# Kernel tuning notes

Measured on AMD Instinct MI355X. Metric: run time of the kernel, lower is better.

## Reference

```python
import jax, jax.numpy as jnp
import numpy as np
import math

DIFF = True   # params['diff'] -> kind='random_walk'
SHIFT = 0.0   # params['shift']
MIN_WINDOW = 10
EPS = 1e-6


def _window_sizes(T):
    ws = []
    cur = math.log10(MIN_WINDOW)
    end = math.log10(T - 1)
    while cur < end:
        w = int(10 ** cur)
        if MIN_WINDOW <= w <= T - 1:
            ws.append(w)
        cur += 0.25
    if T not in ws:
        ws.append(T)
    return sorted(set(ws))


def _hurst_random_walk(x):
    B, T = x.shape
    ws = _window_sizes(T)  # static python list (shapes are static)
    rs_list = []
    for w in ws:
        n = T // w
        seg = x[:, : n * w].reshape(B, n, w)            # (B, n, w)
        d = seg[..., 1:] - seg[..., :-1]                # (B, n, w-1)
        mean_inc = (seg[..., -1] - seg[..., 0]) / (w - 1)
        dev = d - mean_inc[..., None]
        Z = jnp.cumsum(dev, axis=-1)                    # rescaled-range scan
        R = jnp.max(Z, axis=-1) - jnp.min(Z, axis=-1)   # (B, n)
        S = jnp.std(d, axis=-1, ddof=1)                 # unbiased std
        rs_list.append(jnp.mean(R / (S + EPS), axis=-1))
    RS = jnp.stack(rs_list, axis=1)                     # (B, K)
    X = jnp.log10(jnp.asarray(ws, dtype=x.dtype) + EPS) # (K,)
    Y = jnp.log10(RS + EPS)
    Xc = X - jnp.mean(X)
    denom = jnp.sum(Xc * Xc)
    H = jnp.sum((Y - jnp.mean(Y, axis=1, keepdims=True)) * Xc, axis=1) / (denom + EPS)
    H = jnp.where(jnp.isfinite(H), H, jnp.asarray(1.0, x.dtype))
    return H


def setup_inputs() -> dict:
    key = jax.random.key(0)
    x = jax.random.normal(key, (8192, 4096), dtype=jnp.float32)
    return {"x": x}


def reference(x):
    H = _hurst_random_walk(x)
    return (H + SHIFT)[:, None]  # (B, 1)
```

## Files before the change

### kernel.cpp

```cpp
#include <hip/hip_runtime.h>
#include <math.h>
#include <utility>

#define TLEN 4096
#define NW   12
#define BLOCK 256
#define EPSF 1e-6f

typedef float v2f __attribute__((ext_vector_type(2)));

__device__ const float XC_TAB[NW] = {
    -1.3608041f, -1.1303552f, -0.8694424f, -0.6126161f,
    -0.3608041f, -0.1128308f,  0.1388830f,  0.3889322f,
     0.6391959f,  0.8891277f,  1.1391578f,  1.2515558f };
__device__ const float INVN_TAB[NW] = {
    1.0f/409.0f, 1.0f/240.0f, 1.0f/132.0f, 1.0f/73.0f,
    1.0f/40.0f,  1.0f/23.0f,  1.0f/12.0f,  1.0f/7.0f,
    0.25f, 0.5f, 1.0f, 1.0f };
#define INV_DEN 0.11577579f
#define LOG10_2 0.30102999566f

__device__ __forceinline__ float max3f(float a, float b, float c) {
    float r; asm("v_max3_f32 %0, %1, %2, %3" : "=v"(r) : "v"(a), "v"(b), "v"(c)); return r;
}
__device__ __forceinline__ float min3f(float a, float b, float c) {
    float r; asm("v_min3_f32 %0, %1, %2, %3" : "=v"(r) : "v"(a), "v"(b), "v"(c)); return r;
}
__device__ __forceinline__ v2f pk_fma(v2f a, v2f b, v2f c) {
    v2f d; asm("v_pk_fma_f32 %0, %1, %2, %3" : "=v"(d) : "v"(a), "v"(b), "v"(c)); return d;
}
__device__ __forceinline__ v2f pk_add(v2f a, v2f b) {
    v2f d; asm("v_pk_add_f32 %0, %1, %2" : "=v"(d) : "v"(a), "v"(b)); return d;
}

__device__ __forceinline__ float wave_reduce_sum(float v) {
    #pragma unroll
    for (int o = 32; o > 0; o >>= 1) v += __shfl_xor(v, o, 64);
    return v;
}
template<int G>
__device__ __forceinline__ float reduce_leaders(float v) {
    #pragma unroll
    for (int o = G; o < 64; o <<= 1) v += __shfl_xor(v, o, 64);
    return v;
}

template<int FLO, int FHI>
__device__ __forceinline__ float seg_rs2(const float* __restrict__ row,
                                         const float* __restrict__ P4,
                                         int b, int W, float m, float invwm2,
                                         float mx, float mn) {
    float plo = P4[b >> 2];
    if constexpr (FLO > 0) {
        const int k0 = b - FLO;
        #pragma unroll
        for (int t = 0; t < FLO; ++t) {
            float d = row[k0 + t + 1] - row[k0 + t];
            plo = fmaf(d, d, plo);
        }
    }
    const int e = b + W - 1;
    float phi = P4[e >> 2];
    if constexpr (FHI > 0) {
        const int k0 = e - FHI;
        #pragma unroll
        for (int t = 0; t < FHI; ++t) {
            float d = row[k0 + t + 1] - row[k0 + t];
            phi = fmaf(d, d, phi);
        }
    }
    float ss  = phi - plo;
    float var = fmaf(-(float)(W - 1) * m, m, ss) * invwm2;
    float S   = __builtin_amdgcn_sqrtf(fmaxf(var, 0.0f));
    return (mx - mn) * __builtin_amdgcn_rcpf(S + EPSF);
}

template<int LO, int HI, int JB>
__device__ __forceinline__ void chunk_fold(const float4 q, float nm, float& mx, float& mn) {
    if constexpr (LO <= HI) {
        constexpr int NV = HI - LO + 1;
        float v[NV];
        #pragma unroll
        for (int r = 0; r < NV; ++r)
            v[r] = fmaf((float)(JB + LO + r), nm, (&q.x)[LO + r]);
        if constexpr (NV == 1) { mx = fmaxf(mx, v[0]); mn = fminf(mn, v[0]); }
        else if constexpr (NV == 2) { mx = max3f(mx, v[0], v[1]); mn = min3f(mn, v[0], v[1]); }
        else if constexpr (NV == 3) { mx = fmaxf(mx, max3f(v[0], v[1], v[2]));
                                      mn = fminf(mn, min3f(v[0], v[1], v[2])); }
        else { mx = max3f(max3f(mx, v[0], v[1]), v[2], v[3]);
               mn = min3f(min3f(mn, v[0], v[1]), v[2], v[3]); }
    }
}

__device__ __forceinline__ float w10_task(const float* __restrict__ row,
                                          const float* __restrict__ P4,
                                          int t, bool pair) {
    const int b = t * 20;
    const int h = t * 5;
    const float4* p = (const float4*)(row + b);
    float4 q0 = p[0], q1 = p[1], q2 = p[2];
    float acc;
    {
        const float m = (q2.y - q0.x) * (1.0f / 9.0f), nm = -m;
        float v1 = fmaf(1.0f, nm, q0.y);
        float v2 = fmaf(2.0f, nm, q0.z);
        float v3 = fmaf(3.0f, nm, q0.w);
        float mx = max3f(v1, v2, v3), mn = min3f(v1, v2, v3);
        float v4 = fmaf(4.0f, nm, q1.x);
        float v5 = fmaf(5.0f, nm, q1.y);
        float v6 = fmaf(6.0f, nm, q1.z);
        float v7 = fmaf(7.0f, nm, q1.w);
        mx = max3f(mx, v4, v5); mn = min3f(mn, v4, v5);
        mx = max3f(mx, v6, v7); mn = min3f(mn, v6, v7);
        float v8 = fmaf(8.0f, nm, q2.x);
        float v9 = fmaf(9.0f, nm, q2.y);
        mx = max3f(mx, v8, v9); mn = min3f(mn, v8, v9);
        float d8 = q2.y - q2.x;
        float ss = fmaf(d8, d8, P4[h + 2]) - P4[h];
        float var = fmaf(-9.0f * m, m, ss) * 0.125f;
        float S = __builtin_amdgcn_sqrtf(fmaxf(var, 0.0f));
        acc = (mx - mn) * __builtin_amdgcn_rcpf(S + EPSF);
    }
    if (pair) {
        float4 q3 = p[3], q4 = p[4];
        const float m = (q4.w - q2.z) * (1.0f / 9.0f), nm = -m;
        float v1 = fmaf(1.0f, nm, q2.w);
        float v2 = fmaf(2.0f, nm, q3.x);
        float v3 = fmaf(3.0f, nm, q3.y);
        float mx = max3f(v1, v2, v3), mn = min3f(v1, v2, v3);
        float v4 = fmaf(4.0f, nm, q3.z);
        float v5 = fmaf(5.0f, nm, q3.w);
        float v6 = fmaf(6.0f, nm, q4.x);
        float v7 = fmaf(7.0f, nm, q4.y);
        mx = max3f(mx, v4, v5); mn = min3f(mn, v4, v5);
        mx = max3f(mx, v6, v7); mn = min3f(mn, v6, v7);
        float v8 = fmaf(8.0f, nm, q4.z);
        float v9 = fmaf(9.0f, nm, q4.w);
        mx = max3f(mx, v8, v9); mn = min3f(mn, v8, v9);
        float d8  = q2.y - q2.x;
        float d9  = q2.z - q2.y;
        float d16 = q4.y - q4.x;
        float d17 = q4.z - q4.y;
        float d18 = q4.w - q4.z;
        float plo = fmaf(d9, d9, fmaf(d8, d8, P4[h + 2]));
        float phi = fmaf(d18, d18, fmaf(d17, d17, fmaf(d16, d16, P4[h + 4])));
        float ss = phi - plo;
        float var = fmaf(-9.0f * m, m, ss) * 0.125f;
        float S = __builtin_amdgcn_sqrtf(fmaxf(var, 0.0f));
        acc += (mx - mn) * __builtin_amdgcn_rcpf(S + EPSF);
    }
    return acc;
}

template<int W, int NSEG, int C>
__device__ __forceinline__ void mchunk_step(const float4* __restrict__ p,
                                            const float (&nm)[NSEG],
                                            float (&mx)[NSEG], float (&mn)[NSEG]) {
    constexpr int E0 = 4 * C;
    constexpr int K0 = E0 / W;
    constexpr int SA = K0 * W;
    constexpr int LOA = (SA == E0) ? 1 : 0;
    constexpr int HIA_ = SA + W - 1 - E0;
    constexpr int HIA = HIA_ < 3 ? HIA_ : 3;
    float4 q = p[C];
    if constexpr (K0 < NSEG)
        chunk_fold<LOA, HIA, E0 - SA>(q, nm[K0], mx[K0], mn[K0]);
    constexpr bool HASB = (K0 + 1 < NSEG) && (SA + W + 1 - E0 <= 3);
    if constexpr (HASB) {
        constexpr int SB = SA + W;
        chunk_fold<SB + 1 - E0, 3, E0 - SB>(q, nm[K0 + 1], mx[K0 + 1], mn[K0 + 1]);
    }
}

template<int W, int NSEG, int... Cs>
__device__ __forceinline__ void mseg_all(const float4* __restrict__ p,
                                         const float (&nm)[NSEG],
                                         float (&mx)[NSEG], float (&mn)[NSEG],
                                         std::integer_sequence<int, Cs...>) {
    (mchunk_step<W, NSEG, Cs>(p, nm, mx, mn), ...);
}

template<int W, int NSEG, int... Ks>
__device__ __forceinline__ float mseg_rs_all(const float* __restrict__ row,
                                             const float* __restrict__ P4, int b,
                                             const float (&m)[NSEG],
                                             const float (&mx)[NSEG], const float (&mn)[NSEG],
                                             std::integer_sequence<int, Ks...>) {
    constexpr float invwm2 = 1.0f / (float)(W - 2);
    float acc = 0.0f;
    ((acc += seg_rs2<(W * Ks) & 3, (W * Ks + W - 1) & 3>(
          row, P4, b + Ks * W, W, m[Ks], invwm2, mx[Ks], mn[Ks])), ...);
    return acc;
}

template<int W, int NSEG>
__device__ __forceinline__ float mseg_task_odd(const float* __restrict__ row,
                                               const float* __restrict__ P4, int b) {
    constexpr int NCH = (W * NSEG + 3) / 4;
    const float4* p = (const float4*)(row + b);
    float nm[NSEG], m[NSEG], mx[NSEG], mn[NSEG];
    #pragma unroll
    for (int k = 0; k < NSEG; ++k) {
        float a0 = row[b + k * W];
        float a1 = row[b + k * W + W - 1];
        m[k] = (a1 - a0) * (1.0f / (float)(W - 1));
        nm[k] = -m[k];
        mx[k] = -INFINITY; mn[k] = INFINITY;
    }
    mseg_all<W, NSEG>(p, nm, mx, mn, std::make_integer_sequence<int, NCH>{});
    return mseg_rs_all<W, NSEG>(row, P4, b, m, mx, mn,
                                std::make_integer_sequence<int, NSEG>{});
}

template<int W, int A, int G>
__device__ __forceinline__ void seg_strided_pk(const float* __restrict__ row, int b, int lane,
                                               float nm, float& mx, float& mn) {
    constexpr int NCH  = (A + W - 1) / 4 + 1;
    constexpr int HIL  = (A + W - 1) & 3;
    constexpr int MAIN_END = (HIL == 3) ? NCH : NCH - 1;
    constexpr int NFULL = MAIN_END - 1;
    constexpr int FULL  = NFULL / G;
    constexpr int REM   = NFULL % G;
    constexpr int NB    = FULL + (REM > 0 ? 1 : 0);
    const float4* p  = (const float4*)(row + (b - A));
    const float4* pl = p + (1 + lane);
    float4 qs[NB > 0 ? NB : 1];
    #pragma unroll
    for (int i = 0; i < FULL; ++i) qs[i] = pl[i * G];
    if constexpr (REM > 0) { if (lane < REM) qs[FULL] = pl[FULL * G]; }
    mx = -INFINITY; mn = INFINITY;
    v2f jc; jc.x = (float)(4 * (1 + lane) - A); jc.y = jc.x + 1.0f;
    const v2f nm2   = {nm, nm};
    const v2f nm2x2 = {nm + nm, nm + nm};
    const v2f step  = {(float)(4 * G), (float)(4 * G)};
    #pragma unroll
    for (int i = 0; i < FULL; ++i) {
        float4 q = qs[i];
        v2f q01 = {q.x, q.y}, q23 = {q.z, q.w};
        v2f t01 = pk_fma(jc, nm2, q01);
        v2f t23 = pk_fma(jc, nm2, pk_add(q23, nm2x2));
        mx = max3f(max3f(mx, t01.x, t01.y), t23.x, t23.y);
        mn = min3f(min3f(mn, t01.x, t01.y), t23.x, t23.y);
        jc = pk_add(jc, step);
    }
    if constexpr (REM > 0) {
        if (lane < REM) {
            float4 q = qs[FULL];
            v2f q01 = {q.x, q.y}, q23 = {q.z, q.w};
            v2f t01 = pk_fma(jc, nm2, q01);
            v2f t23 = pk_fma(jc, nm2, pk_add(q23, nm2x2));
            mx = max3f(max3f(mx, t01.x, t01.y), t23.x, t23.y);
            mn = min3f(min3f(mn, t01.x, t01.y), t23.x, t23.y);
        }
    }
    if constexpr (A < 3) {
        if (lane == 0) chunk_fold<A + 1, 3, -A>(p[0], nm, mx, mn);
    }
    if constexpr (HIL != 3) {
        if (lane == 1) chunk_fold<0, HIL, 4 * (NCH - 1) - A>(p[NCH - 1], nm, mx, mn);
    }
}

template<int W, int A, int G>
__device__ __forceinline__ float group_seg(const float* __restrict__ row,
                                           const float* __restrict__ P4,
                                           int s, int lane) {
    const int b = s * W;
    float a0 = row[b], a1 = row[b + W - 1];
    float m = (a1 - a0) * (1.0f / (float)(W - 1));
    float nm = -m;
    float mx, mn;
    seg_strided_pk<W, A, G>(row, b, lane, nm, mx, mn);
    #pragma unroll
    for (int o = G / 2; o > 0; o >>= 1) {
        mx = fmaxf(mx, __shfl_xor(mx, o, G));
        mn = fminf(mn, __shfl_xor(mn, o, G));
    }
    float r = seg_rs2<A, (A + W - 1) & 3>(
        row, P4, b, W, m, 1.0f / (float)(W - 2), mx, mn);
    return (lane == 0) ? r : 0.0f;
}

__global__ __launch_bounds__(BLOCK, 7) void hurst_kernel(const float* __restrict__ x,
                                                         float* __restrict__ out) {
    __shared__ __align__(16) float row[TLEN];
    __shared__ __align__(16) float P4[TLEN / 4];
    __shared__ float rs_sum[NW];
    __shared__ float wred[8];

    const int tid = threadIdx.x;
    const int r = blockIdx.x;
    const int w = tid >> 6, l = tid & 63;

    const float4* src = (const float4*)(x + (size_t)r * TLEN);
    float4* dst = (float4*)row;
    #pragma unroll
    for (int i = 0; i < TLEN / 4 / BLOCK; ++i)
        dst[tid + i * BLOCK] = src[tid + i * BLOCK];
    if (tid < NW) rs_sum[tid] = 0.0f;
    __syncthreads();

    {
        const int base = tid * 16;
        float v[17];
        const float4* rp = (const float4*)(row + base);
        float4 q0 = rp[0], q1 = rp[1], q2 = rp[2], q3 = rp[3];
        v[0]=q0.x;  v[1]=q0.y;  v[2]=q0.z;  v[3]=q0.w;
        v[4]=q1.x;  v[5]=q1.y;  v[6]=q1.z;  v[7]=q1.w;
        v[8]=q2.x;  v[9]=q2.y;  v[10]=q2.z; v[11]=q2.w;
        v[12]=q3.x; v[13]=q3.y; v[14]=q3.z; v[15]=q3.w;
        v[16] = row[(base + 16 < TLEN) ? base + 16 : TLEN - 1];

        float pl4[4];
        float c = 0.0f;
        #pragma unroll
        for (int j = 0; j < 16; ++j) {
            if ((j & 3) == 0) pl4[j >> 2] = c;
            float d = v[j + 1] - v[j];
            c = fmaf(d, d, c);
        }
        const float total = c;
        float incl = total;
        #pragma unroll
        for (int o = 1; o < 64; o <<= 1) {
            float u = __shfl_up(incl, o, 64);
            if (l >= o) incl += u;
        }
        if (l == 63) wred[w] = incl;
        __syncthreads();
        float off = incl - total;
        #pragma unroll
        for (int w2 = 0; w2 < 4; ++w2)
            if (w2 < w) off += wred[w2];
        float4* pp = (float4*)(P4 + tid * 4);
        pp[0] = make_float4(off + pl4[0], off + pl4[1], off + pl4[2], off + pl4[3]);
    }
    __syncthreads();


    {
        float a = 0.0f;
        if (tid < 204)       a = w10_task(row, P4, tid, true);
        else if (tid == 204) a = w10_task(row, P4, 204, false);
        a = wave_reduce_sum(a);
        if (l == 0) atomicAdd(&rs_sum[0], a);
    }
    if (w == 0) {
        float a = (l < 60) ? mseg_task_odd<17, 4>(row, P4, l * 68) : 0.0f;
        a = wave_reduce_sum(a);
        if (l == 0) atomicAdd(&rs_sum[1], a);
    } else if (w == 1) {
        float a = (l < 33) ? mseg_task_odd<31, 4>(row, P4, l * 124) : 0.0f;
        a = wave_reduce_sum(a);
        if (l == 0) atomicAdd(&rs_sum[2], a);
    }
    {
        const int g = tid >> 2, gl = tid & 3;
        float a = group_seg<56, 0, 4>(row, P4, g, gl);
        if (w == 2) {
            int s2 = 64 + ((tid - 128) >> 2);
            if (s2 < 73) a += group_seg<56, 0, 4>(row, P4, s2, gl);
        }
        a = reduce_leaders<4>(a);
        if (l == 0) atomicAdd(&rs_sum[3], a);
    }
    {
        const int g = tid >> 3, gl = tid & 7;
        float a = group_seg<100, 0, 8>(row, P4, g, gl);
        if (w == 3)
            a += group_seg<100, 0, 8>(row, P4, 32 + ((tid - 192) >> 3), gl);
        a = reduce_leaders<8>(a);
        if (l == 0) atomicAdd(&rs_sum[4], a);
    }
    {
        const int g4 = (tid >> 4) & 3, gl16 = tid & 15;
        float a = 0.0f;
        if (w == 0) {
            a = group_seg<177, 0, 16>(row, P4, 4 * g4, gl16);
            if (g4 < 2) a += group_seg<177, 0, 16>(row, P4, 4 * (g4 + 4), gl16);
        } else if (w == 1) {
            a = group_seg<177, 1, 16>(row, P4, 4 * g4 + 1, gl16);
            if (g4 < 2) a += group_seg<177, 1, 16>(row, P4, 4 * (g4 + 4) + 1, gl16);
        } else if (w == 2) {
            a = group_seg<177, 2, 16>(row, P4, 4 * g4 + 2, gl16);
            if (g4 < 2) a += group_seg<177, 2, 16>(row, P4, 4 * (g4 + 4) + 2, gl16);
        } else {
            a = group_seg<177, 3, 16>(row, P4, 4 * g4 + 3, gl16);
            if (g4 < 1) a += group_seg<177, 3, 16>(row, P4, 4 * (g4 + 4) + 3, gl16);
        }
        a = reduce_leaders<16>(a);
        if (l == 0) atomicAdd(&rs_sum[5], a);
    }
    if (w != 1) {
        const int g4 = (tid >> 4) & 3, gl16 = tid & 15;
        const int base = (w == 0) ? 0 : (w == 2) ? 4 : 8;
        float a = group_seg<316, 0, 16>(row, P4, base + g4, gl16);
        a = reduce_leaders<16>(a);
        if (l == 0) atomicAdd(&rs_sum[6], a);
    }
    {
        const int gh = (tid >> 5) & 1, gl32 = tid & 31;
        if (w == 2) {
            float a = group_seg<562, 0, 32>(row, P4, 2 * gh, gl32);
            a += group_seg<562, 0, 32>(row, P4, 4 + 2 * gh, gl32);
            a = reduce_leaders<32>(a);
            if (l == 0) atomicAdd(&rs_sum[7], a);
        } else if (w == 3) {
            float a = group_seg<562, 2, 32>(row, P4, 1 + 2 * gh, gl32);
            if (gh == 0) a += group_seg<562, 2, 32>(row, P4, 5, gl32);
            a = reduce_leaders<32>(a);
            if (l == 0) atomicAdd(&rs_sum[7], a);
        }
    }
    if (w >= 2) {
        const int gh = (tid >> 5) & 1, gl32 = tid & 31;
        const int s = (w == 2 ? 0 : 2) + gh;
        float a = group_seg<1000, 0, 32>(row, P4, s, gl32);
        a = reduce_leaders<32>(a);
        if (l == 0) atomicAdd(&rs_sum[8], a);
    }


    {
        const int half = tid >> 7, hl = tid & 127;
        const int b = half ? 1778 : 0;
        float m = (row[b + 1777] - row[b]) * (1.0f / 1777.0f);
        float nm = -m, mx, mn;
        if (half == 0) seg_strided_pk<1778, 0, 128>(row, 0,    hl, nm, mx, mn);
        else           seg_strided_pk<1778, 2, 128>(row, 1778, hl, nm, mx, mn);
        #pragma unroll
        for (int o = 32; o > 0; o >>= 1) {
            mx = fmaxf(mx, __shfl_xor(mx, o, 64));
            mn = fminf(mn, __shfl_xor(mn, o, 64));
        }
        if (l == 0) { wred[w * 2] = mx; wred[w * 2 + 1] = mn; }
        __syncthreads();
        if ((tid & 127) == 0) {
            const int wb = tid >> 6;
            float MX = fmaxf(wred[wb * 2],     wred[wb * 2 + 2]);
            float MN = fminf(wred[wb * 2 + 1], wred[wb * 2 + 3]);
            float v;
            if (tid == 0) v = seg_rs2<0, 1>(row, P4, 0,    1778, m, 1.0f / 1776.0f, MX, MN);
            else          v = seg_rs2<2, 3>(row, P4, 1778, 1778, m, 1.0f / 1776.0f, MX, MN);
            atomicAdd(&rs_sum[9], v);
        }
        __syncthreads();
    }
    {
        float m = (row[3161] - row[0]) * (1.0f / 3161.0f);
        float nm = -m, mx, mn;
        seg_strided_pk<3162, 0, 256>(row, 0, tid, nm, mx, mn);
        #pragma unroll
        for (int o = 32; o > 0; o >>= 1) {
            mx = fmaxf(mx, __shfl_xor(mx, o, 64));
            mn = fminf(mn, __shfl_xor(mn, o, 64));
        }
        if (l == 0) { wred[w * 2] = mx; wred[w * 2 + 1] = mn; }
        __syncthreads();
        if (tid == 0) {
            float MX = fmaxf(fmaxf(wred[0], wred[2]), fmaxf(wred[4], wred[6]));
            float MN = fminf(fminf(wred[1], wred[3]), fminf(wred[5], wred[7]));
            atomicAdd(&rs_sum[10],
                      seg_rs2<0, 1>(row, P4, 0, 3162, m, 1.0f / 3160.0f, MX, MN));
        }
        __syncthreads();
    }
    {
        float m = (row[4095] - row[0]) * (1.0f / 4095.0f);
        float nm = -m, mx, mn;
        seg_strided_pk<4096, 0, 256>(row, 0, tid, nm, mx, mn);
        #pragma unroll
        for (int o = 32; o > 0; o >>= 1) {
            mx = fmaxf(mx, __shfl_xor(mx, o, 64));
            mn = fminf(mn, __shfl_xor(mn, o, 64));
        }
        if (l == 0) { wred[w * 2] = mx; wred[w * 2 + 1] = mn; }
        __syncthreads();
        if (tid == 0) {
            float MX = fmaxf(fmaxf(wred[0], wred[2]), fmaxf(wred[4], wred[6]));
            float MN = fminf(fminf(wred[1], wred[3]), fminf(wred[5], wred[7]));
            atomicAdd(&rs_sum[11],
                      seg_rs2<0, 3>(row, P4, 0, 4096, m, 1.0f / 4094.0f, MX, MN));
        }
        __syncthreads();
    }

    if (tid < 64) {
        float t = 0.0f;
        if (tid < NW) {
            float rs = fmaf(rs_sum[tid], INVN_TAB[tid], EPSF);
            t = __builtin_amdgcn_logf(rs) * (LOG10_2) * XC_TAB[tid];
        }
        t = wave_reduce_sum(t);
        if (tid == 0) {
            float h = t * INV_DEN;
            if (!isfinite(h)) h = 1.0f;
            out[r] = h;
        }
    }
}

extern "C" void kernel_launch(void* const* d_in, const int* in_sizes, int n_in,
                              void* d_out, int out_size, void* d_ws, size_t ws_size,
                              hipStream_t stream) {
    const float* x = (const float*)d_in[0];
    float* out = (float*)d_out;
    const int B = out_size;
    hipLaunchKernelGGL(hurst_kernel, dim3(B), dim3(BLOCK), 0, stream, x, out);
}
```

Before: 90.05 us.

## Fuse window-10 R/S into prefix pass and rebalance segment work across waves

Each of 205 threads now handles a 20-element span and builds the prefix sums. The window-10 rescaled ranges are computed from those same registers during that pass, removing the separate w10 pass and its reads back from shared memory. The prefix-sum layout changes from 16 to 20 elements per thread, which leaves 51 threads idle during the prefix phase. Window-31 work is split across two waves with a base-offset template, and the window-316/562/1000/100/56 leftover segments are redistributed per wave to balance load. This costs more divergent, wave-specific code.

```diff
diff --git a/kernel.cpp b/kernel.cpp
--- a/kernel.cpp
+++ b/kernel.cpp
@@ -92,112 +92,59 @@
     }
 }
 
-__device__ __forceinline__ float w10_task(const float* __restrict__ row,
-                                          const float* __restrict__ P4,
-                                          int t, bool pair) {
-    const int b = t * 20;
-    const int h = t * 5;
-    const float4* p = (const float4*)(row + b);
-    float4 q0 = p[0], q1 = p[1], q2 = p[2];
-    float acc;
-    {
-        const float m = (q2.y - q0.x) * (1.0f / 9.0f), nm = -m;
-        float v1 = fmaf(1.0f, nm, q0.y);
-        float v2 = fmaf(2.0f, nm, q0.z);
-        float v3 = fmaf(3.0f, nm, q0.w);
-        float mx = max3f(v1, v2, v3), mn = min3f(v1, v2, v3);
-        float v4 = fmaf(4.0f, nm, q1.x);
-        float v5 = fmaf(5.0f, nm, q1.y);
-        float v6 = fmaf(6.0f, nm, q1.z);
-        float v7 = fmaf(7.0f, nm, q1.w);
-        mx = max3f(mx, v4, v5); mn = min3f(mn, v4, v5);
-        mx = max3f(mx, v6, v7); mn = min3f(mn, v6, v7);
-        float v8 = fmaf(8.0f, nm, q2.x);
-        float v9 = fmaf(9.0f, nm, q2.y);
-        mx = max3f(mx, v8, v9); mn = min3f(mn, v8, v9);
-        float d8 = q2.y - q2.x;
-        float ss = fmaf(d8, d8, P4[h + 2]) - P4[h];
-        float var = fmaf(-9.0f * m, m, ss) * 0.125f;
-        float S = __builtin_amdgcn_sqrtf(fmaxf(var, 0.0f));
-        acc = (mx - mn) * __builtin_amdgcn_rcpf(S + EPSF);
-    }
-    if (pair) {
-        float4 q3 = p[3], q4 = p[4];
-        const float m = (q4.w - q2.z) * (1.0f / 9.0f), nm = -m;
-        float v1 = fmaf(1.0f, nm, q2.w);
-        float v2 = fmaf(2.0f, nm, q3.x);
-        float v3 = fmaf(3.0f, nm, q3.y);
-        float mx = max3f(v1, v2, v3), mn = min3f(v1, v2, v3);
-        float v4 = fmaf(4.0f, nm, q3.z);
-        float v5 = fmaf(5.0f, nm, q3.w);
-        float v6 = fmaf(6.0f, nm, q4.x);
-        float v7 = fmaf(7.0f, nm, q4.y);
-        mx = max3f(mx, v4, v5); mn = min3f(mn, v4, v5);
-        mx = max3f(mx, v6, v7); mn = min3f(mn, v6, v7);
-        float v8 = fmaf(8.0f, nm, q4.z);
-        float v9 = fmaf(9.0f, nm, q4.w);
-        mx = max3f(mx, v8, v9); mn = min3f(mn, v8, v9);
-        float d8  = q2.y - q2.x;
-        float d9  = q2.z - q2.y;
-        float d16 = q4.y - q4.x;
-        float d17 = q4.z - q4.y;
-        float d18 = q4.w - q4.z;
-        float plo = fmaf(d9, d9, fmaf(d8, d8, P4[h + 2]));
-        float phi = fmaf(d18, d18, fmaf(d17, d17, fmaf(d16, d16, P4[h + 4])));
-        float ss = phi - plo;
-        float var = fmaf(-9.0f * m, m, ss) * 0.125f;
-        float S = __builtin_amdgcn_sqrtf(fmaxf(var, 0.0f));
-        acc += (mx - mn) * __builtin_amdgcn_rcpf(S + EPSF);
-    }
-    return acc;
-}
-
-template<int W, int NSEG, int C>
-__device__ __forceinline__ void mchunk_step(const float4* __restrict__ p,
-                                            const float (&nm)[NSEG],
-                                            float (&mx)[NSEG], float (&mn)[NSEG]) {
-    constexpr int E0 = 4 * C;
-    constexpr int K0 = E0 / W;
-    constexpr int SA = K0 * W;
-    constexpr int LOA = (SA == E0) ? 1 : 0;
-    constexpr int HIA_ = SA + W - 1 - E0;
-    constexpr int HIA = HIA_ < 3 ? HIA_ : 3;
+template<int W, int NSEG, int BP, int C>
+__device__ __forceinline__ void mchunk_stepA(const float4* __restrict__ p,
+                                             const float (&nm)[NSEG],
+                                             float (&mx)[NSEG], float (&mn)[NSEG]) {
     float4 q = p[C];
-    if constexpr (K0 < NSEG)
-        chunk_fold<LOA, HIA, E0 - SA>(q, nm[K0], mx[K0], mn[K0]);
-    constexpr bool HASB = (K0 + 1 < NSEG) && (SA + W + 1 - E0 <= 3);
-    if constexpr (HASB) {
+    if constexpr (C == 0 && BP > 0) {
+        chunk_fold<BP + 1, 3, -BP>(q, nm[0], mx[0], mn[0]);
+    } else {
+        constexpr int E0 = 4 * C - BP;
+        constexpr int K0 = E0 / W;
+        constexpr int SA = K0 * W;
+        constexpr int LOA = (SA == E0) ? 1 : 0;
+        constexpr int HIA1 = SA + W - 1 - E0;
+        constexpr int HIA2 = NSEG * W - 1 - E0;
+        constexpr int HIA = (3 < HIA1 ? (3 < HIA2 ? 3 : HIA2) : (HIA1 < HIA2 ? HIA1 : HIA2));
+        if constexpr (K0 < NSEG)
+            chunk_fold<LOA, HIA, E0 - SA>(q, nm[K0], mx[K0], mn[K0]);
         constexpr int SB = SA + W;
-        chunk_fold<SB + 1 - E0, 3, E0 - SB>(q, nm[K0 + 1], mx[K0 + 1], mn[K0 + 1]);
-    }
-}
-
-template<int W, int NSEG, int... Cs>
-__device__ __forceinline__ void mseg_all(const float4* __restrict__ p,
-                                         const float (&nm)[NSEG],
-                                         float (&mx)[NSEG], float (&mn)[NSEG],
-                                         std::integer_sequence<int, Cs...>) {
-    (mchunk_step<W, NSEG, Cs>(p, nm, mx, mn), ...);
-}
-
-template<int W, int NSEG, int... Ks>
-__device__ __forceinline__ float mseg_rs_all(const float* __restrict__ row,
-                                             const float* __restrict__ P4, int b,
-                                             const float (&m)[NSEG],
-                                             const float (&mx)[NSEG], const float (&mn)[NSEG],
-                                             std::integer_sequence<int, Ks...>) {
+        constexpr bool HASB = (K0 + 1 < NSEG) && (SB + 1 - E0 <= 3);
+        if constexpr (HASB) {
+            constexpr int HIB2 = NSEG * W - 1 - E0;
+            constexpr int HIB = (3 < HIB2 ? 3 : HIB2);
+            chunk_fold<SB + 1 - E0, HIB, E0 - SB>(q, nm[K0 + 1], mx[K0 + 1], mn[K0 + 1]);
+        }
+    }
+}
+
+template<int W, int NSEG, int BP, int... Cs>
+__device__ __forceinline__ void mseg_allA(const float4* __restrict__ p,
+                                          const float (&nm)[NSEG],
+                                          float (&mx)[NSEG], float (&mn)[NSEG],
+                                          std::integer_sequence<int, Cs...>) {
+    (mchunk_stepA<W, NSEG, BP, Cs>(p, nm, mx, mn), ...);
+}
+
+template<int W, int NSEG, int BP, int... Ks>
+__device__ __forceinline__ float mseg_rs_allA(const float* __restrict__ row,
+                                              const float* __restrict__ P4, int b,
+                                              const float (&m)[NSEG],
+                                              const float (&mx)[NSEG], const float (&mn)[NSEG],
+                                              std::integer_sequence<int, Ks...>) {
     constexpr float invwm2 = 1.0f / (float)(W - 2);
     float acc = 0.0f;
-    ((acc += seg_rs2<(W * Ks) & 3, (W * Ks + W - 1) & 3>(
+    ((acc += seg_rs2<(BP + W * Ks) & 3, (BP + W * Ks + W - 1) & 3>(
           row, P4, b + Ks * W, W, m[Ks], invwm2, mx[Ks], mn[Ks])), ...);
     return acc;
 }
 
-template<int W, int NSEG>
-__device__ __forceinline__ float mseg_task_odd(const float* __restrict__ row,
-                                               const float* __restrict__ P4, int b) {
-    constexpr int NCH = (W * NSEG + 3) / 4;
-    const float4* p = (const float4*)(row + b);
+template<int W, int NSEG, int BP>
+__device__ __forceinline__ float mseg_task_a(const float* __restrict__ row,
+                                             const float* __restrict__ P4, int b) {
+    constexpr int NCH = (BP + W * NSEG + 3) / 4;
+    const float4* p = (const float4*)(row + b - BP);
     float nm[NSEG], m[NSEG], mx[NSEG], mn[NSEG];
     #pragma unroll
     for (int k = 0; k < NSEG; ++k) {
@@ -207,9 +154,9 @@
         nm[k] = -m[k];
         mx[k] = -INFINITY; mn[k] = INFINITY;
     }
-    mseg_all<W, NSEG>(p, nm, mx, mn, std::make_integer_sequence<int, NCH>{});
-    return mseg_rs_all<W, NSEG>(row, P4, b, m, mx, mn,
-                                std::make_integer_sequence<int, NSEG>{});
+    mseg_allA<W, NSEG, BP>(p, nm, mx, mn, std::make_integer_sequence<int, NCH>{});
+    return mseg_rs_allA<W, NSEG, BP>(row, P4, b, m, mx, mn,
+                                     std::make_integer_sequence<int, NSEG>{});
 }
 
 template<int W, int A, int G>
@@ -281,6 +228,27 @@
     return (lane == 0) ? r : 0.0f;
 }
 
+template<int B, int NV>
+__device__ __forceinline__ float w10_seg(const float (&v)[NV], float ss) {
+    const float m = (v[B + 9] - v[B]) * (1.0f / 9.0f), nm = -m;
+    float x1 = fmaf(1.0f, nm, v[B + 1]);
+    float x2 = fmaf(2.0f, nm, v[B + 2]);
+    float x3 = fmaf(3.0f, nm, v[B + 3]);
+    float x4 = fmaf(4.0f, nm, v[B + 4]);
+    float x5 = fmaf(5.0f, nm, v[B + 5]);
+    float x6 = fmaf(6.0f, nm, v[B + 6]);
+    float x7 = fmaf(7.0f, nm, v[B + 7]);
+    float x8 = fmaf(8.0f, nm, v[B + 8]);
+    float x9 = fmaf(9.0f, nm, v[B + 9]);
+    float mx = max3f(x1, x2, x3);
+    mx = max3f(mx, x4, x5); mx = max3f(mx, x6, x7); mx = max3f(mx, x8, x9);
+    float mn = min3f(x1, x2, x3);
+    mn = min3f(mn, x4, x5); mn = min3f(mn, x6, x7); mn = min3f(mn, x8, x9);
+    float var = fmaf(-9.0f * m, m, ss) * 0.125f;
+    float S = __builtin_amdgcn_sqrtf(fmaxf(var, 0.0f));
+    return (mx - mn) * __builtin_amdgcn_rcpf(S + EPSF);
+}
+
 __global__ __launch_bounds__(BLOCK, 7) void hurst_kernel(const float* __restrict__ x,
                                                          float* __restrict__ out) {
     __shared__ __align__(16) float row[TLEN];
@@ -301,25 +269,44 @@
     __syncthreads();
 
     {
-        const int base = tid * 16;
-        float v[17];
-        const float4* rp = (const float4*)(row + base);
-        float4 q0 = rp[0], q1 = rp[1], q2 = rp[2], q3 = rp[3];
-        v[0]=q0.x;  v[1]=q0.y;  v[2]=q0.z;  v[3]=q0.w;
-        v[4]=q1.x;  v[5]=q1.y;  v[6]=q1.z;  v[7]=q1.w;
-        v[8]=q2.x;  v[9]=q2.y;  v[10]=q2.z; v[11]=q2.w;
-        v[12]=q3.x; v[13]=q3.y; v[14]=q3.z; v[15]=q3.w;
-        v[16] = row[(base + 16 < TLEN) ? base + 16 : TLEN - 1];
-
-        float pl4[4];
-        float c = 0.0f;
-        #pragma unroll
-        for (int j = 0; j < 16; ++j) {
-            if ((j & 3) == 0) pl4[j >> 2] = c;
-            float d = v[j + 1] - v[j];
-            c = fmaf(d, d, c);
-        }
-        const float total = c;
+        float total = 0.0f;
+        float lp[5] = {0, 0, 0, 0, 0};
+        float contrib = 0.0f;
+        if (tid < 204) {
+            const int b = tid * 20;
+            const float4* p = (const float4*)(row + b);
+            float4 q0 = p[0], q1 = p[1], q2 = p[2], q3 = p[3], q4 = p[4];
+            float v[21] = {q0.x,q0.y,q0.z,q0.w, q1.x,q1.y,q1.z,q1.w,
+                           q2.x,q2.y,q2.z,q2.w, q3.x,q3.y,q3.z,q3.w,
+                           q4.x,q4.y,q4.z,q4.w, row[b + 20]};
+            float c = 0.0f, s9 = 0.0f, s10 = 0.0f, s19 = 0.0f;
+            #pragma unroll
+            for (int j = 0; j < 20; ++j) {
+                if ((j & 3) == 0) lp[j >> 2] = c;
+                if (j == 9)  s9  = c;
+                if (j == 10) s10 = c;
+                if (j == 19) s19 = c;
+                float d = v[j + 1] - v[j];
+                c = fmaf(d, d, c);
+            }
+            total = c;
+            contrib = w10_seg<0>(v, s9) + w10_seg<10>(v, s19 - s10);
+        } else if (tid == 204) {
+            const float4* p = (const float4*)(row + 4080);
+            float4 q0 = p[0], q1 = p[1], q2 = p[2], q3 = p[3];
+            float v[16] = {q0.x,q0.y,q0.z,q0.w, q1.x,q1.y,q1.z,q1.w,
+                           q2.x,q2.y,q2.z,q2.w, q3.x,q3.y,q3.z,q3.w};
+            float c = 0.0f, s9 = 0.0f;
+            #pragma unroll
+            for (int j = 0; j < 15; ++j) {
+                if ((j & 3) == 0) lp[j >> 2] = c;
+                if (j == 9) s9 = c;
+                float d = v[j + 1] - v[j];
+                c = fmaf(d, d, c);
+            }
+            total = c;
+            contrib = w10_seg<0>(v, s9);
+        }
         float incl = total;
         #pragma unroll
         for (int o = 1; o < 64; o <<= 1) {
@@ -327,48 +314,32 @@
             if (l >= o) incl += u;
         }
         if (l == 63) wred[w] = incl;
+        float a = wave_reduce_sum(contrib);
+        if (l == 0) atomicAdd(&rs_sum[0], a);
         __syncthreads();
         float off = incl - total;
         #pragma unroll
         for (int w2 = 0; w2 < 4; ++w2)
             if (w2 < w) off += wred[w2];
-        float4* pp = (float4*)(P4 + tid * 4);
-        pp[0] = make_float4(off + pl4[0], off + pl4[1], off + pl4[2], off + pl4[3]);
-    }
-    __syncthreads();
-
-
-    {
-        float a = 0.0f;
-        if (tid < 204)       a = w10_task(row, P4, tid, true);
-        else if (tid == 204) a = w10_task(row, P4, 204, false);
-        a = wave_reduce_sum(a);
-        if (l == 0) atomicAdd(&rs_sum[0], a);
-    }
-    if (w == 0) {
-        float a = (l < 60) ? mseg_task_odd<17, 4>(row, P4, l * 68) : 0.0f;
-        a = wave_reduce_sum(a);
-        if (l == 0) atomicAdd(&rs_sum[1], a);
-    } else if (w == 1) {
-        float a = (l < 33) ? mseg_task_odd<31, 4>(row, P4, l * 124) : 0.0f;
-        a = wave_reduce_sum(a);
-        if (l == 0) atomicAdd(&rs_sum[2], a);
-    }
-    {
-        const int g = tid >> 2, gl = tid & 3;
-        float a = group_seg<56, 0, 4>(row, P4, g, gl);
-        if (w == 2) {
-            int s2 = 64 + ((tid - 128) >> 2);
-            if (s2 < 73) a += group_seg<56, 0, 4>(row, P4, s2, gl);
-        }
+        if (tid < 204) {
+            const int h = tid * 5;
+            #pragma unroll
+            for (int c2 = 0; c2 < 5; ++c2) P4[h + c2] = off + lp[c2];
+        } else if (tid == 204) {
+            #pragma unroll
+            for (int c2 = 0; c2 < 4; ++c2) P4[1020 + c2] = off + lp[c2];
+        }
+        __syncthreads();
+    }
+
+
+    {
+        float a = group_seg<56, 0, 4>(row, P4, tid >> 2, tid & 3);
         a = reduce_leaders<4>(a);
         if (l == 0) atomicAdd(&rs_sum[3], a);
     }
     {
-        const int g = tid >> 3, gl = tid & 7;
-        float a = group_seg<100, 0, 8>(row, P4, g, gl);
-        if (w == 3)
-            a += group_seg<100, 0, 8>(row, P4, 32 + ((tid - 192) >> 3), gl);
+        float a = group_seg<100, 0, 8>(row, P4, tid >> 3, tid & 7);
         a = reduce_leaders<8>(a);
         if (l == 0) atomicAdd(&rs_sum[4], a);
     }
@@ -391,33 +362,48 @@
         a = reduce_leaders<16>(a);
         if (l == 0) atomicAdd(&rs_sum[5], a);
     }
-    if (w != 1) {
-        const int g4 = (tid >> 4) & 3, gl16 = tid & 15;
-        const int base = (w == 0) ? 0 : (w == 2) ? 4 : 8;
-        float a = group_seg<316, 0, 16>(row, P4, base + g4, gl16);
-        a = reduce_leaders<16>(a);
-        if (l == 0) atomicAdd(&rs_sum[6], a);
-    }
-    {
-        const int gh = (tid >> 5) & 1, gl32 = tid & 31;
-        if (w == 2) {
-            float a = group_seg<562, 0, 32>(row, P4, 2 * gh, gl32);
-            a += group_seg<562, 0, 32>(row, P4, 4 + 2 * gh, gl32);
-            a = reduce_leaders<32>(a);
-            if (l == 0) atomicAdd(&rs_sum[7], a);
-        } else if (w == 3) {
-            float a = group_seg<562, 2, 32>(row, P4, 1 + 2 * gh, gl32);
-            if (gh == 0) a += group_seg<562, 2, 32>(row, P4, 5, gl32);
-            a = reduce_leaders<32>(a);
-            if (l == 0) atomicAdd(&rs_sum[7], a);
-        }
-    }
-    if (w >= 2) {
-        const int gh = (tid >> 5) & 1, gl32 = tid & 31;
-        const int s = (w == 2 ? 0 : 2) + gh;
-        float a = group_seg<1000, 0, 32>(row, P4, s, gl32);
-        a = reduce_leaders<32>(a);
-        if (l == 0) atomicAdd(&rs_sum[8], a);
+
+    if (w == 0) {
+        float a = (l < 60) ? mseg_task_a<17, 4, 0>(row, P4, l * 68) : 0.0f;
+        a = wave_reduce_sum(a);
+        if (l == 0) atomicAdd(&rs_sum[1], a);
+        float c1 = group_seg<316, 0, 16>(row, P4, 4 + ((l >> 4) & 3), l & 15);
+        c1 += group_seg<316, 0, 16>(row, P4, 8 + ((l >> 4) & 3), l & 15);
+        c1 = reduce_leaders<16>(c1);
+        if (l == 0) atomicAdd(&rs_sum[6], c1);
+        float c2 = group_seg<100, 0, 8>(row, P4, 32 + (l >> 3), l & 7);
+        c2 = reduce_leaders<8>(c2);
+        if (l == 0) atomicAdd(&rs_sum[4], c2);
+    } else if (w == 1) {
+        float a = (l < 33) ? mseg_task_a<31, 2, 0>(row, P4, 124 * l) : 0.0f;
+        a = wave_reduce_sum(a);
+        if (l == 0) atomicAdd(&rs_sum[2], a);
+        float c1 = group_seg<562, 2, 32>(row, P4, 1 + 2 * (l >> 5), l & 31);
+        c1 = reduce_leaders<32>(c1);
+        if (l == 0) atomicAdd(&rs_sum[7], c1);
+        float c2 = ((l >> 2) < 9) ? group_seg<56, 0, 4>(row, P4, 64 + (l >> 2), l & 3) : 0.0f;
+        c2 = reduce_leaders<4>(c2);
+        if (l == 0) atomicAdd(&rs_sum[3], c2);
+    } else if (w == 2) {
+        float a = (l < 33) ? mseg_task_a<31, 2, 2>(row, P4, 124 * l + 62) : 0.0f;
+        a = wave_reduce_sum(a);
+        if (l == 0) atomicAdd(&rs_sum[2], a);
+        float c1 = group_seg<1000, 0, 32>(row, P4, l >> 5, l & 31);
+        c1 = reduce_leaders<32>(c1);
+        if (l == 0) atomicAdd(&rs_sum[8], c1);
+    } else {
+        float c1 = group_seg<562, 0, 32>(row, P4, 2 * (l >> 5), l & 31);
+        c1 += group_seg<562, 0, 32>(row, P4, 4 + 2 * (l >> 5), l & 31);
+        float c2 = (l < 32) ? group_seg<562, 2, 32>(row, P4, 5, l & 31) : 0.0f;
+        c1 += c2;
+        c1 = reduce_leaders<32>(c1);
+        if (l == 0) atomicAdd(&rs_sum[7], c1);
+        float c3 = group_seg<1000, 0, 32>(row, P4, 2 + (l >> 5), l & 31);
+        c3 = reduce_leaders<32>(c3);
+        if (l == 0) atomicAdd(&rs_sum[8], c3);
+        float c4 = group_seg<316, 0, 16>(row, P4, (l >> 4) & 3, l & 15);
+        c4 = reduce_leaders<16>(c4);
+        if (l == 0) atomicAdd(&rs_sum[6], c4);
     }
 
 
```

Result: faster. 87.29 us (-3.1%).
